# Kernel optimization log

Measured on AMD Instinct MI355X. Metric: run time of the kernel, lower is better.

## Reference

```python
import jax, jax.numpy as jnp
import numpy as np
import math

B, L, E, H, K = 4, 1024, 1024, 16, 64
D = E // H  # head_dim = 64; rel_pe has 2K+1 = 129 rows


def setup_inputs() -> dict:
    key = jax.random.key(0)
    ks = jax.random.split(key, 4)
    s = 1.0 / math.sqrt(E)
    return {
        "q": jax.random.normal(ks[0], (B, L, E), dtype=jnp.float32),
        "in_proj_weight": jax.random.normal(ks[1], (3 * E, E), dtype=jnp.float32) * s,
        "in_proj_bias": jnp.zeros((3 * E,), dtype=jnp.float32),
        "out_w": jax.random.normal(ks[2], (E, E), dtype=jnp.float32) * s,
        "out_b": jnp.zeros((E,), dtype=jnp.float32),
        "rel_pe": jax.random.normal(ks[3], (2 * K + 1, D), dtype=jnp.float32) * (1.0 / math.sqrt(D)),
    }


def _attend(q, in_proj_weight, in_proj_bias, out_w, out_b, rel_pe):
    b, l, e = q.shape
    h, d = H, D
    qkv = q @ in_proj_weight.T + in_proj_bias  # (B, L, 3E)
    qh, kh, vh = jnp.split(qkv, 3, axis=-1)
    # (B, L, E) -> (B, H, L, D)
    qh = qh.reshape(b, l, h, d).transpose(0, 2, 1, 3)
    kh = kh.reshape(b, l, h, d).transpose(0, 2, 1, 3)
    vh = vh.reshape(b, l, h, d).transpose(0, 2, 1, 3)
    qh = qh / math.sqrt(d)  # scaling applies to both content and position terms
    # content scores
    scores = jnp.einsum("bhid,bhjd->bhij", qh, kh)
    # relative-position bias: a[i, j] = rel_pe[clip(j - i, -K, K) + K]
    # compute q . rel_pe once, then gather per (i, j) -- same math as the
    # original O(L^2 * D) materialized tensor, without building it.
    pos = jnp.arange(l)
    rel = jnp.clip(pos[None, :] - pos[:, None], -K, K) + K  # (L, L) int
    bias_r = jnp.einsum("bhid,rd->bhir", qh, rel_pe)  # (B, H, L, 2K+1)
    bias = jnp.take_along_axis(bias_r, jnp.broadcast_to(rel[None, None], (b, h, l, l)), axis=-1)
    attn = jax.nn.softmax(scores + bias, axis=-1)
    out = jnp.einsum("bhij,bhjd->bhid", attn, vh)  # (B, H, L, D)
    out = out.transpose(0, 2, 1, 3).reshape(b, l, e)
    return out @ out_w.T + out_b


def reference(q, in_proj_weight, in_proj_bias, out_w, out_b, rel_pe):
    return _attend(q, in_proj_weight, in_proj_bias, out_w, out_b, rel_pe)
```

## Files before the change

### kernel.cpp

```cpp
#include <hip/hip_runtime.h>
#include <math.h>

typedef _Float16 half_t;
typedef _Float16 half8 __attribute__((ext_vector_type(8)));
typedef _Float16 half4v __attribute__((ext_vector_type(4)));
typedef float float4v __attribute__((ext_vector_type(4)));
typedef float float16v __attribute__((ext_vector_type(16)));

#define AS1 __attribute__((address_space(1)))
#define AS3 __attribute__((address_space(3)))

#define MFMA16(a, b, c) __builtin_amdgcn_mfma_f32_16x16x32_f16((a), (b), (c), 0, 0, 0)
#define MFMA32(a, b, c) __builtin_amdgcn_mfma_f32_32x32x16_f16((a), (b), (c), 0, 0, 0)

#define QSCALE 0.18033688f
#define TABOFF 2.88539008f

__device__ __forceinline__ void gload16(const half_t* g, half_t* l) {
    __builtin_amdgcn_global_load_lds((const AS1 void*)g, (AS3 void*)l, 16, 0, 0);
}

__device__ __forceinline__ int iclamp(int v, int lo, int hi) {
    return v < lo ? lo : (v > hi ? hi : v);
}

__device__ __forceinline__ unsigned pkrtz_bits(float a, float b) {
    auto w = __builtin_amdgcn_cvt_pkrtz(a, b);
    unsigned u;
    __builtin_memcpy(&u, &w, 4);
    return u;
}

__device__ __forceinline__ void softmax_pack(const float16v* s, float4v& lacc,
                                             half8* pf) {
    unsigned pw[2][4][2];
#pragma unroll
    for (int t2 = 0; t2 < 2; ++t2)
#pragma unroll
        for (int g = 0; g < 4; ++g) {
            float p0 = __builtin_amdgcn_exp2f(s[t2][4 * g + 0]);
            float p1 = __builtin_amdgcn_exp2f(s[t2][4 * g + 1]);
            float p2 = __builtin_amdgcn_exp2f(s[t2][4 * g + 2]);
            float p3 = __builtin_amdgcn_exp2f(s[t2][4 * g + 3]);
            lacc += (float4v){p0, p1, p2, p3};
            pw[t2][g][0] = pkrtz_bits(p0, p1);
            pw[t2][g][1] = pkrtz_bits(p2, p3);
        }
#pragma unroll
    for (int cc = 0; cc < 4; ++cc) {
        const int t2c = cc >> 1, ge = (cc & 1) * 2;
        auto r0 = __builtin_amdgcn_permlane32_swap(
            pw[t2c][ge][0], pw[t2c][ge + 1][0], false, false);
        auto r1 = __builtin_amdgcn_permlane32_swap(
            pw[t2c][ge][1], pw[t2c][ge + 1][1], false, false);
        unsigned pfw[4] = {r0[0], r1[0], r0[1], r1[1]};
        __builtin_memcpy(&pf[cc], pfw, 16);
    }
}

__device__ __forceinline__ void bias_init(int kt64, int i0w, int i0w_s, int hl,
                                          int hiC, const half_t* r2row,
                                          float c_lo, float c_hi, float16v* s) {
    if (kt64 >= i0w_s + 95) {
#pragma unroll
        for (int t2 = 0; t2 < 2; ++t2)
#pragma unroll
            for (int r = 0; r < 16; ++r) s[t2][r] = c_hi;
    } else if (kt64 <= i0w_s - 127) {
#pragma unroll
        for (int t2 = 0; t2 < 2; ++t2)
#pragma unroll
            for (int r = 0; r < 16; ++r) s[t2][r] = c_lo;
    } else {
#pragma unroll
        for (int t2 = 0; t2 < 2; ++t2)
#pragma unroll
            for (int g = 0; g < 4; ++g) {
                int traw = kt64 + t2 * 32 + 8 * g + 4 * hl + 64 - i0w;
                int tsb = iclamp(traw, -4, hiC) + 4;
                half4v bh4 = *(const half4v*)(r2row + tsb);
#pragma unroll
                for (int r = 0; r < 4; ++r) s[t2][4 * g + r] = (float)bh4[r];
            }
    }
}

__global__ __launch_bounds__(256) void cast_kernel(
    const float* __restrict__ q, const float* __restrict__ w_in,
    const float* __restrict__ w_out, const float* __restrict__ pe,
    half_t* __restrict__ q16, half_t* __restrict__ w16,
    half_t* __restrict__ wo16, half_t* __restrict__ pe16)
{
    const int tid = blockIdx.x * 256 + threadIdx.x;
    const int stride = gridDim.x * 256;
    for (int i = tid; i < 1048576; i += stride) {
        float4 v = ((const float4*)q)[i];
        *(half4v*)(q16 + (size_t)i * 4) =
            (half4v){(half_t)v.x, (half_t)v.y, (half_t)v.z, (half_t)v.w};
    }
    for (int i = tid; i < 786432; i += stride) {
        float4 v = ((const float4*)w_in)[i];
        *(half4v*)(w16 + (size_t)i * 4) =
            (half4v){(half_t)v.x, (half_t)v.y, (half_t)v.z, (half_t)v.w};
    }
    for (int i = tid; i < 262144; i += stride) {
        float4 v = ((const float4*)w_out)[i];
        *(half4v*)(wo16 + (size_t)i * 4) =
            (half4v){(half_t)v.x, (half_t)v.y, (half_t)v.z, (half_t)v.w};
    }
    for (int i = tid; i < 2064; i += stride) {
        float4 v = ((const float4*)pe)[i];
        *(half4v*)(pe16 + (size_t)i * 4) =
            (half4v){(half_t)v.x, (half_t)v.y, (half_t)v.z, (half_t)v.w};
    }
    for (int i = tid; i < 496; i += stride) {
        *(half4v*)(pe16 + 8256 + (size_t)i * 4) = (half4v){0, 0, 0, 0};
    }
}

__global__ __launch_bounds__(256) void qkv_gemm(
    const half_t* __restrict__ A, const half_t* __restrict__ W,
    const float* __restrict__ bias,
    half_t* __restrict__ qh, half_t* __restrict__ kh, half_t* __restrict__ vt)
{
    __shared__ half_t As[128 * 32];
    __shared__ half_t Bs[128 * 32];
    const int K = 1024;
    const int tid = threadIdx.x, lane = tid & 63, wid = tid >> 6;
    const int wm = wid & 1, wn = wid >> 1;
    const int bid = blockIdx.x;
    const int xcd = bid & 7, idx = bid >> 3;
    const int m0 = (((xcd >> 1) << 3) + (idx & 7)) * 128;
    const int n0 = (((xcd & 1) * 12) + (idx >> 3)) * 128;

    const half_t* gA[2]; const half_t* gB[2];
    half_t* lA[2]; half_t* lB[2];
    {
        const int base = wid * 128;
#pragma unroll
        for (int c = 0; c < 2; ++c) {
            int slot = base + c * 64 + lane;
            int row = slot >> 2;
            int ch = (slot & 3) ^ ((row >> 1) & 3);
            gA[c] = A + (size_t)(m0 + row) * K + ch * 8;
            gB[c] = W + (size_t)(n0 + row) * K + ch * 8;
            lA[c] = As + (base + c * 64) * 8;
            lB[c] = Bs + (base + c * 64) * 8;
        }
    }
    int aOff[4], bOff[4];
#pragma unroll
    for (int i = 0; i < 4; ++i) {
        int ra = wm * 64 + i * 16 + (lane & 15);
        aOff[i] = ra * 32 + (((lane >> 4) ^ ((ra >> 1) & 3)) * 8);
        int rb = wn * 64 + i * 16 + (lane & 15);
        bOff[i] = rb * 32 + (((lane >> 4) ^ ((rb >> 1) & 3)) * 8);
    }
    float4v acc[4][4];
#pragma unroll
    for (int i = 0; i < 4; ++i)
#pragma unroll
        for (int j = 0; j < 4; ++j) acc[i][j] = (float4v){0.f, 0.f, 0.f, 0.f};

    for (int k0 = 0; k0 < K; k0 += 32) {
        __syncthreads();
        gload16(gA[0], lA[0]); gload16(gA[1], lA[1]);
        gload16(gB[0], lB[0]); gload16(gB[1], lB[1]);
        gA[0] += 32; gA[1] += 32; gB[0] += 32; gB[1] += 32;
        __syncthreads();
        half8 af[4], bf[4];
#pragma unroll
        for (int i = 0; i < 4; ++i) af[i] = *(const half8*)(As + aOff[i]);
#pragma unroll
        for (int j = 0; j < 4; ++j) bf[j] = *(const half8*)(Bs + bOff[j]);
#pragma unroll
        for (int i = 0; i < 4; ++i)
#pragma unroll
            for (int j = 0; j < 4; ++j)
                acc[i][j] = MFMA16(af[i], bf[j], acc[i][j]);
    }

    const int part = n0 >> 10;
#pragma unroll
    for (int ni = 0; ni < 4; ++ni) {
        const int col = n0 + wn * 64 + ni * 16 + (lane & 15);
        const float bv = bias[col];
        const int hh = (col >> 6) & 15, d = col & 63;
#pragma unroll
        for (int mi = 0; mi < 4; ++mi) {
            const int r0 = m0 + wm * 64 + mi * 16 + ((lane >> 4) << 2);
            const int bb = r0 >> 10, l0 = r0 & 1023;
            if (part == 0) {
#pragma unroll
                for (int r = 0; r < 4; ++r)
                    qh[(((size_t)(bb * 16 + hh) * 1024) + l0 + r) * 64 + d] =
                        (half_t)((acc[mi][ni][r] + bv) * QSCALE);
            } else if (part == 1) {
#pragma unroll
                for (int r = 0; r < 4; ++r)
                    kh[(((size_t)(bb * 16 + hh) * 1024) + l0 + r) * 64 + d] =
                        (half_t)(acc[mi][ni][r] + bv);
            } else {
                half4v pk;
#pragma unroll
                for (int r = 0; r < 4; ++r) pk[r] = (half_t)(acc[mi][ni][r] + bv);
                *(half4v*)(vt + ((size_t)(bb * 16 + hh) * 64 + d) * 1024 + l0) = pk;
            }
        }
    }
}

__global__ __launch_bounds__(256) void out_gemm(
    const half_t* __restrict__ A, const half_t* __restrict__ W,
    const float* __restrict__ bias, float* __restrict__ C)
{
    __shared__ half_t As[128 * 32];
    __shared__ half_t Bs[64 * 32];
    const int K = 1024;
    const int tid = threadIdx.x, lane = tid & 63, wid = tid >> 6;
    const int wm = wid & 1, wn = wid >> 1;
    const int bid = blockIdx.x;
    const int xcd = bid & 7, idx = bid >> 3;
    const int m0 = ((xcd << 2) + (idx >> 4)) * 128;
    const int n0 = (idx & 15) * 64;

    const half_t* gA[2]; const half_t* gB1;
    half_t* lA[2]; half_t* lB1;
    {
        const int base = wid * 128;
#pragma unroll
        for (int c = 0; c < 2; ++c) {
            int slot = base + c * 64 + lane;
            int row = slot >> 2;
            int ch = (slot & 3) ^ ((row >> 1) & 3);
            gA[c] = A + (size_t)(m0 + row) * K + ch * 8;
            lA[c] = As + (base + c * 64) * 8;
        }
        int slotB = wid * 64 + lane;
        int rowB = slotB >> 2;
        int chB = (slotB & 3) ^ ((rowB >> 1) & 3);
        gB1 = W + (size_t)(n0 + rowB) * K + chB * 8;
        lB1 = Bs + (wid * 64) * 8;
    }
    int aOff[4], bOff[2];
#pragma unroll
    for (int i = 0; i < 4; ++i) {
        int ra = wm * 64 + i * 16 + (lane & 15);
        aOff[i] = ra * 32 + (((lane >> 4) ^ ((ra >> 1) & 3)) * 8);
    }
#pragma unroll
    for (int j = 0; j < 2; ++j) {
        int rb = wn * 32 + j * 16 + (lane & 15);
        bOff[j] = rb * 32 + (((lane >> 4) ^ ((rb >> 1) & 3)) * 8);
    }
    float4v acc[4][2];
#pragma unroll
    for (int i = 0; i < 4; ++i)
#pragma unroll
        for (int j = 0; j < 2; ++j) acc[i][j] = (float4v){0.f, 0.f, 0.f, 0.f};

    for (int k0 = 0; k0 < K; k0 += 32) {
        __syncthreads();
        gload16(gA[0], lA[0]); gload16(gA[1], lA[1]);
        gload16(gB1, lB1);
        gA[0] += 32; gA[1] += 32; gB1 += 32;
        __syncthreads();
        half8 af[4], bf[2];
#pragma unroll
        for (int i = 0; i < 4; ++i) af[i] = *(const half8*)(As + aOff[i]);
#pragma unroll
        for (int j = 0; j < 2; ++j) bf[j] = *(const half8*)(Bs + bOff[j]);
#pragma unroll
        for (int i = 0; i < 4; ++i)
#pragma unroll
            for (int j = 0; j < 2; ++j)
                acc[i][j] = MFMA16(af[i], bf[j], acc[i][j]);
    }

#pragma unroll
    for (int ni = 0; ni < 2; ++ni) {
        const int col = n0 + wn * 32 + ni * 16 + (lane & 15);
        const float bv = bias[col];
#pragma unroll
        for (int mi = 0; mi < 4; ++mi) {
            const int r0 = m0 + wm * 64 + mi * 16 + ((lane >> 4) << 2);
#pragma unroll
            for (int r = 0; r < 4; ++r)
                C[(size_t)(r0 + r) * 1024 + col] = acc[mi][ni][r] + bv;
        }
    }
}

__global__ __launch_bounds__(256) void attn_mfma(
    const half_t* __restrict__ qh, const half_t* __restrict__ kh,
    const half_t* __restrict__ vt, const half_t* __restrict__ pe,
    half_t* __restrict__ ao)
{
    __shared__ half_t KV[2 * 8192];
    __shared__ half_t R2[4 * 32 * 172];

    const int tid = threadIdx.x, lane = tid & 63, wid = tid >> 6;
    const int hl = lane >> 5, ql = lane & 31;
    const int bid = blockIdx.x;
    const int xcd = bid & 7, idx = bid >> 3;
    const int bh = xcd + ((idx >> 3) << 3);
    const int q0 = (idx & 7) * 128;
    const int h = bh & 15, b = bh >> 4;
    const int i0w = q0 + wid * 32;
    const int i0w_s = __builtin_amdgcn_readfirstlane(i0w);
    const size_t hbase = (size_t)(b * 16 + h) * 64 * 1024;
    const half_t* Qg = qh + hbase;
    const half_t* Kg = kh + hbase;
    const half_t* Vg = vt + hbase;

    const half_t* gS[4]; int lOff[4]; int ginc[4];
#pragma unroll
    for (int c = 0; c < 4; ++c) {
        const int slot0 = wid * 256 + c * 64;
        const int slot = slot0 + lane;
        if (slot0 < 512) {
            int srow = slot >> 3, sch = (slot & 7) ^ (srow & 7);
            gS[c] = Kg + srow * 64 + sch * 8;
            ginc[c] = 64 * 64;
            lOff[c] = slot0 * 8;
        } else {
            int s2 = slot - 512;
            int srow = s2 >> 3, sch = (s2 & 7) ^ (srow & 7);
            gS[c] = Vg + srow * 1024 + sch * 8;
            ginc[c] = 64;
            lOff[c] = 4096 + (slot0 - 512) * 8;
        }
    }

#pragma unroll
    for (int c = 0; c < 4; ++c) { gload16(gS[c], KV + lOff[c]); gS[c] += ginc[c]; }
#pragma unroll
    for (int c = 0; c < 4; ++c) { gload16(gS[c], KV + 8192 + lOff[c]); gS[c] += ginc[c]; }

    const int qrow = i0w + ql;
    half8 qb[4];
#pragma unroll
    for (int cc = 0; cc < 4; ++cc)
        qb[cc] = *(const half8*)(Qg + (size_t)qrow * 64 + cc * 16 + hl * 8);

    half_t* r2w = R2 + wid * (32 * 172);
#pragma unroll
    for (int j2 = 0; j2 < 5; ++j2) {
        float16v c;
#pragma unroll
        for (int r = 0; r < 16; ++r) c[r] = 0.f;
#pragma unroll
        for (int cc = 0; cc < 4; ++cc) {
            half8 pb = *(const half8*)(pe + (size_t)(j2 * 32 + ql) * 64 + cc * 16 + hl * 8);
            c = MFMA32(qb[cc], pb, c);
        }
        const int col = j2 * 32 + ql;
        if (col < 129) {
#pragma unroll
            for (int reg = 0; reg < 16; ++reg) {
                const int il = (reg & 3) + 8 * (reg >> 2) + 4 * hl;
                const half_t hv = (half_t)(c[reg] - TABOFF);
                if (col == 0) {
                    for (int ts = 0; ts <= il + 4; ++ts) r2w[il * 172 + ts] = hv;
                } else if (col == 128) {
                    for (int ts = il + 132; ts <= il + 139; ++ts) r2w[il * 172 + ts] = hv;
                } else {
                    r2w[il * 172 + col + 4 + il] = hv;
                }
            }
        }
    }
    asm volatile("s_waitcnt lgkmcnt(0)" ::: "memory");

    const half_t* r2row = r2w + ql * 172;
    const float c_lo = (float)r2row[0];
    const float c_hi = (float)r2row[ql + 132];
    const int hiC = 128 + ((ql + 3) & ~3);

    int kOff[2][4], vOff[2][4];
#pragma unroll
    for (int t2 = 0; t2 < 2; ++t2)
#pragma unroll
        for (int cc = 0; cc < 4; ++cc) {
            int row = t2 * 32 + ql;
            int ch = (cc * 2 + hl) ^ (row & 7);
            kOff[t2][cc] = row * 64 + ch * 8;
            vOff[t2][cc] = 4096 + row * 64 + ch * 8;
        }

    float4v lacc = (float4v){0.f, 0.f, 0.f, 0.f};
    float16v oacc[2];
#pragma unroll
    for (int dt = 0; dt < 2; ++dt)
#pragma unroll
        for (int r = 0; r < 16; ++r) oacc[dt][r] = 0.f;

    asm volatile("s_waitcnt vmcnt(4)" ::: "memory");
    __builtin_amdgcn_s_barrier();

    half8 pf[4];
    {
        float16v s[2];
        bias_init(0, i0w, i0w_s, hl, hiC, r2row, c_lo, c_hi, s);
#pragma unroll
        for (int t2 = 0; t2 < 2; ++t2)
#pragma unroll
            for (int cc = 0; cc < 4; ++cc) {
                half8 kf = *(const half8*)(KV + kOff[t2][cc]);
                s[t2] = MFMA32(kf, qb[cc], s[t2]);
            }
        softmax_pack(s, lacc, pf);
    }

    for (int kt = 0; kt < 16; ++kt) {
        asm volatile("s_waitcnt vmcnt(0)" ::: "memory");
        __builtin_amdgcn_s_barrier();

        const half_t* bufN = KV + (((kt + 1) & 1) << 13);
        const half_t* bufC = KV + ((kt & 1) << 13);
        const bool hasn = kt < 15;

        float16v s[2];
        if (hasn) {
            bias_init((kt + 1) << 6, i0w, i0w_s, hl, hiC, r2row, c_lo, c_hi, s);
#pragma unroll
            for (int t2 = 0; t2 < 2; ++t2)
#pragma unroll
                for (int cc = 0; cc < 4; ++cc) {
                    half8 kf = *(const half8*)(bufN + kOff[t2][cc]);
                    s[t2] = MFMA32(kf, qb[cc], s[t2]);
                }
        }

#pragma unroll
        for (int dt = 0; dt < 2; ++dt)
#pragma unroll
            for (int cc = 0; cc < 4; ++cc) {
                half8 vf = *(const half8*)(bufC + vOff[dt][cc]);
                oacc[dt] = MFMA32(vf, pf[cc], oacc[dt]);
            }

        asm volatile("s_waitcnt lgkmcnt(0)" ::: "memory");
        __builtin_amdgcn_s_barrier();

        if (kt < 14) {
#pragma unroll
            for (int c = 0; c < 4; ++c) {
                gload16(gS[c], KV + ((kt & 1) << 13) + lOff[c]);
                gS[c] += ginc[c];
            }
        }

        if (hasn) softmax_pack(s, lacc, pf);
    }

    float l_r = lacc[0] + lacc[1] + lacc[2] + lacc[3];
    l_r += __shfl_xor(l_r, 32);
    const float inv = 1.0f / l_r;

    half_t* aorow = ao + ((size_t)(b * 1024 + i0w + ql)) * 1024 + h * 64;
#pragma unroll
    for (int dt = 0; dt < 2; ++dt)
#pragma unroll
        for (int g = 0; g < 4; ++g) {
            const int d0 = dt * 32 + 8 * g + 4 * hl;
            half4v oh;
#pragma unroll
            for (int r = 0; r < 4; ++r) oh[r] = (half_t)(oacc[dt][4 * g + r] * inv);
            *(half4v*)(aorow + d0) = oh;
        }
}

extern "C" void kernel_launch(void* const* d_in, const int* in_sizes, int n_in,
                              void* d_out, int out_size, void* d_ws, size_t ws_size,
                              hipStream_t stream) {
    const float* q     = (const float*)d_in[0];
    const float* w_in  = (const float*)d_in[1];
    const float* b_in  = (const float*)d_in[2];
    const float* w_out = (const float*)d_in[3];
    const float* b_out = (const float*)d_in[4];
    const float* pe    = (const float*)d_in[5];
    float* out = (float*)d_out;

    half_t* ws = (half_t*)d_ws;
    half_t* q16   = ws;
    half_t* w16   = q16 + 4194304;
    half_t* wo16  = w16 + 3145728;
    half_t* pe16  = wo16 + 1048576;
    half_t* qh16  = pe16 + 10240;
    half_t* kh16  = qh16 + 4194304;
    half_t* vt16  = kh16 + 4194304;
    half_t* ao16  = vt16 + 4194304;

    cast_kernel<<<2048, 256, 0, stream>>>(q, w_in, w_out, pe, q16, w16, wo16, pe16);
    qkv_gemm<<<768, 256, 0, stream>>>(q16, w16, b_in, qh16, kh16, vt16);
    attn_mfma<<<512, 256, 0, stream>>>(qh16, kh16, vt16, pe16, ao16);
    out_gemm<<<512, 256, 0, stream>>>(ao16, wo16, b_out, out);
}
```

Baseline: 193.6 us.

## Double-buffer GEMM LDS tiles and restructure attention K/V prefetch pipeline

```diff
diff --git a/kernel.cpp b/kernel.cpp
--- a/kernel.cpp
+++ b/kernel.cpp
@@ -123,8 +123,8 @@
     const float* __restrict__ bias,
     half_t* __restrict__ qh, half_t* __restrict__ kh, half_t* __restrict__ vt)
 {
-    __shared__ half_t As[128 * 32];
-    __shared__ half_t Bs[128 * 32];
+    __shared__ half_t As[2][128 * 32];
+    __shared__ half_t Bs[2][128 * 32];
     const int K = 1024;
     const int tid = threadIdx.x, lane = tid & 63, wid = tid >> 6;
     const int wm = wid & 1, wn = wid >> 1;
@@ -134,7 +134,7 @@
     const int n0 = (((xcd & 1) * 12) + (idx >> 3)) * 128;
 
     const half_t* gA[2]; const half_t* gB[2];
-    half_t* lA[2]; half_t* lB[2];
+    int lOffA[2], lOffB[2];
     {
         const int base = wid * 128;
 #pragma unroll
@@ -144,8 +144,8 @@
             int ch = (slot & 3) ^ ((row >> 1) & 3);
             gA[c] = A + (size_t)(m0 + row) * K + ch * 8;
             gB[c] = W + (size_t)(n0 + row) * K + ch * 8;
-            lA[c] = As + (base + c * 64) * 8;
-            lB[c] = Bs + (base + c * 64) * 8;
+            lOffA[c] = (base + c * 64) * 8;
+            lOffB[c] = (base + c * 64) * 8;
         }
     }
     int aOff[4], bOff[4];
@@ -162,22 +162,38 @@
 #pragma unroll
         for (int j = 0; j < 4; ++j) acc[i][j] = (float4v){0.f, 0.f, 0.f, 0.f};
 
-    for (int k0 = 0; k0 < K; k0 += 32) {
-        __syncthreads();
-        gload16(gA[0], lA[0]); gload16(gA[1], lA[1]);
-        gload16(gB[0], lB[0]); gload16(gB[1], lB[1]);
-        gA[0] += 32; gA[1] += 32; gB[0] += 32; gB[1] += 32;
-        __syncthreads();
+    gload16(gA[0], &As[0][0] + lOffA[0]); gload16(gA[1], &As[0][0] + lOffA[1]);
+    gload16(gB[0], &Bs[0][0] + lOffB[0]); gload16(gB[1], &Bs[0][0] + lOffB[1]);
+    gA[0] += 32; gA[1] += 32; gB[0] += 32; gB[1] += 32;
+
+    for (int it = 0; it < 32; ++it) {
+        const int cur = it & 1;
+        if (it < 31) {
+            const int nxt = cur ^ 1;
+            gload16(gA[0], &As[nxt][0] + lOffA[0]);
+            gload16(gA[1], &As[nxt][0] + lOffA[1]);
+            gload16(gB[0], &Bs[nxt][0] + lOffB[0]);
+            gload16(gB[1], &Bs[nxt][0] + lOffB[1]);
+            gA[0] += 32; gA[1] += 32; gB[0] += 32; gB[1] += 32;
+            asm volatile("s_waitcnt vmcnt(4)" ::: "memory");
+        } else {
+            asm volatile("s_waitcnt vmcnt(0)" ::: "memory");
+        }
+        __builtin_amdgcn_s_barrier();
+
         half8 af[4], bf[4];
 #pragma unroll
-        for (int i = 0; i < 4; ++i) af[i] = *(const half8*)(As + aOff[i]);
-#pragma unroll
-        for (int j = 0; j < 4; ++j) bf[j] = *(const half8*)(Bs + bOff[j]);
+        for (int i = 0; i < 4; ++i) af[i] = *(const half8*)(&As[cur][0] + aOff[i]);
+#pragma unroll
+        for (int j = 0; j < 4; ++j) bf[j] = *(const half8*)(&Bs[cur][0] + bOff[j]);
 #pragma unroll
         for (int i = 0; i < 4; ++i)
 #pragma unroll
             for (int j = 0; j < 4; ++j)
                 acc[i][j] = MFMA16(af[i], bf[j], acc[i][j]);
+
+        asm volatile("s_waitcnt lgkmcnt(0)" ::: "memory");
+        __builtin_amdgcn_s_barrier();
     }
 
     const int part = n0 >> 10;
@@ -214,8 +230,8 @@
     const half_t* __restrict__ A, const half_t* __restrict__ W,
     const float* __restrict__ bias, float* __restrict__ C)
 {
-    __shared__ half_t As[128 * 32];
-    __shared__ half_t Bs[64 * 32];
+    __shared__ half_t As[2][128 * 32];
+    __shared__ half_t Bs[2][64 * 32];
     const int K = 1024;
     const int tid = threadIdx.x, lane = tid & 63, wid = tid >> 6;
     const int wm = wid & 1, wn = wid >> 1;
@@ -225,7 +241,7 @@
     const int n0 = (idx & 15) * 64;
 
     const half_t* gA[2]; const half_t* gB1;
-    half_t* lA[2]; half_t* lB1;
+    int lOffA[2], lOffB1;
     {
         const int base = wid * 128;
 #pragma unroll
@@ -234,13 +250,13 @@
             int row = slot >> 2;
             int ch = (slot & 3) ^ ((row >> 1) & 3);
             gA[c] = A + (size_t)(m0 + row) * K + ch * 8;
-            lA[c] = As + (base + c * 64) * 8;
+            lOffA[c] = (base + c * 64) * 8;
         }
         int slotB = wid * 64 + lane;
         int rowB = slotB >> 2;
         int chB = (slotB & 3) ^ ((rowB >> 1) & 3);
         gB1 = W + (size_t)(n0 + rowB) * K + chB * 8;
-        lB1 = Bs + (wid * 64) * 8;
+        lOffB1 = (wid * 64) * 8;
     }
     int aOff[4], bOff[2];
 #pragma unroll
@@ -259,22 +275,37 @@
 #pragma unroll
         for (int j = 0; j < 2; ++j) acc[i][j] = (float4v){0.f, 0.f, 0.f, 0.f};
 
-    for (int k0 = 0; k0 < K; k0 += 32) {
-        __syncthreads();
-        gload16(gA[0], lA[0]); gload16(gA[1], lA[1]);
-        gload16(gB1, lB1);
-        gA[0] += 32; gA[1] += 32; gB1 += 32;
-        __syncthreads();
+    gload16(gA[0], &As[0][0] + lOffA[0]); gload16(gA[1], &As[0][0] + lOffA[1]);
+    gload16(gB1, &Bs[0][0] + lOffB1);
+    gA[0] += 32; gA[1] += 32; gB1 += 32;
+
+    for (int it = 0; it < 32; ++it) {
+        const int cur = it & 1;
+        if (it < 31) {
+            const int nxt = cur ^ 1;
+            gload16(gA[0], &As[nxt][0] + lOffA[0]);
+            gload16(gA[1], &As[nxt][0] + lOffA[1]);
+            gload16(gB1, &Bs[nxt][0] + lOffB1);
+            gA[0] += 32; gA[1] += 32; gB1 += 32;
+            asm volatile("s_waitcnt vmcnt(3)" ::: "memory");
+        } else {
+            asm volatile("s_waitcnt vmcnt(0)" ::: "memory");
+        }
+        __builtin_amdgcn_s_barrier();
+
         half8 af[4], bf[2];
 #pragma unroll
-        for (int i = 0; i < 4; ++i) af[i] = *(const half8*)(As + aOff[i]);
-#pragma unroll
-        for (int j = 0; j < 2; ++j) bf[j] = *(const half8*)(Bs + bOff[j]);
+        for (int i = 0; i < 4; ++i) af[i] = *(const half8*)(&As[cur][0] + aOff[i]);
+#pragma unroll
+        for (int j = 0; j < 2; ++j) bf[j] = *(const half8*)(&Bs[cur][0] + bOff[j]);
 #pragma unroll
         for (int i = 0; i < 4; ++i)
 #pragma unroll
             for (int j = 0; j < 2; ++j)
                 acc[i][j] = MFMA16(af[i], bf[j], acc[i][j]);
+
+        asm volatile("s_waitcnt lgkmcnt(0)" ::: "memory");
+        __builtin_amdgcn_s_barrier();
     }
 
 #pragma unroll
@@ -334,8 +365,6 @@
 
 #pragma unroll
     for (int c = 0; c < 4; ++c) { gload16(gS[c], KV + lOff[c]); gS[c] += ginc[c]; }
-#pragma unroll
-    for (int c = 0; c < 4; ++c) { gload16(gS[c], KV + 8192 + lOff[c]); gS[c] += ginc[c]; }
 
     const int qrow = i0w + ql;
     half8 qb[4];
@@ -395,63 +424,50 @@
 #pragma unroll
         for (int r = 0; r < 16; ++r) oacc[dt][r] = 0.f;
 
-    asm volatile("s_waitcnt vmcnt(4)" ::: "memory");
-    __builtin_amdgcn_s_barrier();
-
-    half8 pf[4];
-    {
-        float16v s[2];
-        bias_init(0, i0w, i0w_s, hl, hiC, r2row, c_lo, c_hi, s);
-#pragma unroll
-        for (int t2 = 0; t2 < 2; ++t2)
-#pragma unroll
-            for (int cc = 0; cc < 4; ++cc) {
-                half8 kf = *(const half8*)(KV + kOff[t2][cc]);
-                s[t2] = MFMA32(kf, qb[cc], s[t2]);
+    for (int kt2 = 0; kt2 < 8; ++kt2) {
+#pragma unroll
+        for (int kk = 0; kk < 2; ++kk) {
+            const int kt = kt2 * 2 + kk;
+            if (kt < 15) {
+#pragma unroll
+                for (int c = 0; c < 4; ++c) {
+                    gload16(gS[c], KV + (kk ^ 1) * 8192 + lOff[c]);
+                    gS[c] += ginc[c];
+                }
+                asm volatile("s_waitcnt vmcnt(4)" ::: "memory");
+            } else {
+                asm volatile("s_waitcnt vmcnt(0)" ::: "memory");
             }
-        softmax_pack(s, lacc, pf);
-    }
-
-    for (int kt = 0; kt < 16; ++kt) {
-        asm volatile("s_waitcnt vmcnt(0)" ::: "memory");
-        __builtin_amdgcn_s_barrier();
-
-        const half_t* bufN = KV + (((kt + 1) & 1) << 13);
-        const half_t* bufC = KV + ((kt & 1) << 13);
-        const bool hasn = kt < 15;
-
-        float16v s[2];
-        if (hasn) {
-            bias_init((kt + 1) << 6, i0w, i0w_s, hl, hiC, r2row, c_lo, c_hi, s);
+            __builtin_amdgcn_s_barrier();
+            asm volatile("" ::: "memory");
+
+            const half_t* KVb = KV + kk * 8192;
+            const int kt64 = kt << 6;
+
+            float16v s[2];
+            bias_init(kt64, i0w, i0w_s, hl, hiC, r2row, c_lo, c_hi, s);
 #pragma unroll
             for (int t2 = 0; t2 < 2; ++t2)
 #pragma unroll
                 for (int cc = 0; cc < 4; ++cc) {
-                    half8 kf = *(const half8*)(bufN + kOff[t2][cc]);
+                    half8 kf = *(const half8*)(KVb + kOff[t2][cc]);
                     s[t2] = MFMA32(kf, qb[cc], s[t2]);
                 }
-        }
-
-#pragma unroll
-        for (int dt = 0; dt < 2; ++dt)
-#pragma unroll
-            for (int cc = 0; cc < 4; ++cc) {
-                half8 vf = *(const half8*)(bufC + vOff[dt][cc]);
-                oacc[dt] = MFMA32(vf, pf[cc], oacc[dt]);
-            }
-
-        asm volatile("s_waitcnt lgkmcnt(0)" ::: "memory");
-        __builtin_amdgcn_s_barrier();
-
-        if (kt < 14) {
-#pragma unroll
-            for (int c = 0; c < 4; ++c) {
-                gload16(gS[c], KV + ((kt & 1) << 13) + lOff[c]);
-                gS[c] += ginc[c];
-            }
-        }
-
-        if (hasn) softmax_pack(s, lacc, pf);
+
+            half8 pf[4];
+            softmax_pack(s, lacc, pf);
+
+#pragma unroll
+            for (int dt = 0; dt < 2; ++dt)
+#pragma unroll
+                for (int cc = 0; cc < 4; ++cc) {
+                    half8 vf = *(const half8*)(KVb + vOff[dt][cc]);
+                    oacc[dt] = MFMA32(vf, pf[cc], oacc[dt]);
+                }
+
+            asm volatile("" ::: "memory");
+            __builtin_amdgcn_s_barrier();
+        }
     }
 
     float l_r = lacc[0] + lacc[1] + lacc[2] + lacc[3];
```

Result: no change. 194.1 us (+0.3%).
